# Optimization experiments

Hardware: AMD Instinct MI355X
Metric: run time of the kernel (lower is better)

The kernel has to match this reference:

```python
import jax, jax.numpy as jnp
import numpy as np

N_NODES = 50000
N_EDGES = 600000
D = 128
BN_EPS = 1e-5


def _linear_init(key, fan_in, fan_out):
    # torch nn.Linear default: U(-1/sqrt(fan_in), 1/sqrt(fan_in)) for W and b
    kw, kb = jax.random.split(key)
    bound = 1.0 / np.sqrt(fan_in)
    W = jax.random.uniform(kw, (fan_in, fan_out), minval=-bound, maxval=bound, dtype=jnp.float32)
    b = jax.random.uniform(kb, (fan_out,), minval=-bound, maxval=bound, dtype=jnp.float32)
    return W, b


def setup_inputs() -> dict:
    key = jax.random.key(0)
    ks = jax.random.split(key, 8)
    x = jax.random.normal(ks[0], (N_NODES, D), dtype=jnp.float32)
    edge_index = jax.random.randint(ks[1], (2, N_EDGES), 0, N_NODES, dtype=jnp.int32)
    edge_attr = jax.random.normal(ks[2], (N_EDGES, D), dtype=jnp.float32)
    # MLP: [2D, D, D, D] -> Linear(2D,D)+SiLU+BN, Linear(D,D)+SiLU+BN, Linear(D,D)
    W1, b1 = _linear_init(ks[3], 2 * D, D)
    W2, b2 = _linear_init(ks[4], D, D)
    W3, b3 = _linear_init(ks[5], D, D)
    g1 = jnp.ones((D,), jnp.float32); be1 = jnp.zeros((D,), jnp.float32)
    g2 = jnp.ones((D,), jnp.float32); be2 = jnp.zeros((D,), jnp.float32)
    return {"x": x, "edge_index": edge_index, "edge_attr": edge_attr,
            "W1": W1, "b1": b1, "g1": g1, "be1": be1,
            "W2": W2, "b2": b2, "g2": g2, "be2": be2,
            "W3": W3, "b3": b3}


def _bn(h, gamma, beta):
    # BatchNorm1d in training mode: normalize with batch statistics (biased var)
    mean = jnp.mean(h, axis=0)
    var = jnp.var(h, axis=0)
    return (h - mean) * jax.lax.rsqrt(var + BN_EPS) * gamma + beta


def reference(x, edge_index, edge_attr, W1, b1, g1, be1, W2, b2, g2, be2, W3, b3):
    src = edge_index[0]
    # scatter_add over edges indexed by source node -> [N_NODES, D]
    agg = jax.ops.segment_sum(edge_attr, src, num_segments=x.shape[0])
    h = jnp.concatenate([x, agg], axis=1)  # [N, 2D]
    h = _bn(jax.nn.silu(h @ W1 + b1), g1, be1)
    h = _bn(jax.nn.silu(h @ W2 + b2), g2, be2)
    return h @ W3 + b3
```

## Files before the change

### kernel.cpp

```cpp
#include <hip/hip_runtime.h>
#include <hip/hip_bf16.h>

#define D 128

typedef __attribute__((ext_vector_type(8))) short bfrag;
typedef __attribute__((ext_vector_type(4))) float facc;
typedef __attribute__((ext_vector_type(4))) unsigned int u32x4;
typedef __attribute__((ext_vector_type(2))) unsigned int u32x2;
typedef __attribute__((ext_vector_type(4))) float f32x4;

__device__ __forceinline__ facc mfma16(bfrag a, bfrag b, facc c) {
    return __builtin_amdgcn_mfma_f32_16x16x32_bf16(a, b, c, 0, 0, 0);
}
__device__ __forceinline__ unsigned int bf16_rn(float f) {
    unsigned int u = __float_as_uint(f);
    u += 0x7FFF + ((u >> 16) & 1);
    return u >> 16;
}
__device__ __forceinline__ float bf16_f(unsigned int h) {
    return __uint_as_float(h << 16);
}
__device__ __forceinline__ unsigned int packf(float v) {
    unsigned int hi = bf16_rn(v);
    unsigned int lo = bf16_rn(v - bf16_f(hi));
    return (hi << 16) | lo;
}

__global__ __launch_bounds__(256) void prep_kernel(
    const int* __restrict__ src, int* __restrict__ counts, int nedges,
    const float* __restrict__ x, unsigned int* __restrict__ xp, int n4,
    const float* __restrict__ W1, unsigned short* __restrict__ Wh,
    unsigned short* __restrict__ Wl, int eblk, int sblk) {
    int b = blockIdx.x;
    if (b < eblk) {
        int e = b * 256 + threadIdx.x;
        if (e < nedges) atomicAdd(&counts[src[e]], 1);
    } else if (b < eblk + sblk) {
        int i = (b - eblk) * 256 + threadIdx.x;
        if (i < n4) {
            float4 v = ((const float4*)x)[i];
            uint4 p;
            p.x = packf(v.x);
            p.y = packf(v.y);
            p.z = packf(v.z);
            p.w = packf(v.w);
            ((uint4*)xp)[i] = p;
        }
    } else {
        int j = b - eblk - sblk;
        int k = threadIdx.x;
        float w = W1[(size_t)k * D + j];
        unsigned int hi = bf16_rn(w);
        size_t o = (size_t)((k >> 3) * 128 + j) * 8 + (k & 7);
        Wh[o] = (unsigned short)hi;
        Wl[o] = (unsigned short)bf16_rn(w - bf16_f(hi));
    }
}

#define SCHUNK 2048
__global__ __launch_bounds__(256) void scan1_kernel(
    const int* __restrict__ counts, int* __restrict__ bsum, int n) {
    __shared__ int sd[256];
    const int tid = threadIdx.x;
    const int base = blockIdx.x * SCHUNK + tid * 8;
    int s = 0;
#pragma unroll
    for (int j = 0; j < 8; ++j) {
        int idx = base + j;
        if (idx < n) s += counts[idx];
    }
    sd[tid] = s;
    __syncthreads();
    for (int d2 = 128; d2; d2 >>= 1) {
        if (tid < d2) sd[tid] += sd[tid + d2];
        __syncthreads();
    }
    if (tid == 0) bsum[blockIdx.x] = sd[0];
}
__global__ void scan2_kernel(int* __restrict__ bsum, int nb) {
    int tid = threadIdx.x;
    int v = (tid < nb) ? bsum[tid] : 0;
#pragma unroll
    for (int d2 = 1; d2 < 64; d2 <<= 1) {
        int t = __shfl_up(v, d2);
        if (tid >= d2) v += t;
    }
    if (tid < nb) bsum[tid] = v;
}
__global__ __launch_bounds__(256) void scan3_kernel(
    const int* __restrict__ counts, const int* __restrict__ bsum,
    int* __restrict__ off, int* __restrict__ cur, int n) {
    __shared__ int sd[256];
    const int tid = threadIdx.x;
    const int base = blockIdx.x * SCHUNK + tid * 8;
    int loc[8];
    int s = 0;
#pragma unroll
    for (int j = 0; j < 8; ++j) {
        int idx = base + j;
        int c = (idx < n) ? counts[idx] : 0;
        loc[j] = c;
        s += c;
    }
    sd[tid] = s;
    __syncthreads();
#pragma unroll
    for (int d2 = 1; d2 < 256; d2 <<= 1) {
        int t = (tid >= d2) ? sd[tid - d2] : 0;
        __syncthreads();
        sd[tid] += t;
        __syncthreads();
    }
    int boff = (blockIdx.x == 0) ? 0 : bsum[blockIdx.x - 1];
    int pre = boff + sd[tid] - s;
#pragma unroll
    for (int j = 0; j < 8; ++j) {
        int idx = base + j;
        if (idx < n) {
            off[idx] = pre;
            cur[idx] = pre;
            pre += loc[j];
        }
    }
    if (tid == 255 && base + 8 >= n && n <= blockIdx.x * SCHUNK + SCHUNK)
        off[n] = boff + sd[255];
}

__global__ void fill_kernel(const int* __restrict__ src, int* __restrict__ cur,
                            int* __restrict__ eid, int nedges) {
    int e = blockIdx.x * 256 + threadIdx.x;
    if (e < nedges) {
        int slot = atomicAdd(&cur[src[e]], 1);
        eid[slot] = e;
    }
}

__global__ __launch_bounds__(256) void gather_kernel(
    const float* __restrict__ edge_attr, const int* __restrict__ eid,
    const int* __restrict__ off, unsigned int* __restrict__ aggp, int nnodes) {
    int node = blockIdx.x * 4 + (threadIdx.x >> 6);
    int lane = threadIdx.x & 63;
    if (node >= nnodes) return;
    const int h = lane >> 5;
    const int c = lane & 31;
    int i = off[node];
    const int e = off[node + 1];
    f32x4 acc = {0.f, 0.f, 0.f, 0.f};

    if (i < e && (i & 1)) {
        f32x4 v = __builtin_nontemporal_load(
            (const f32x4*)(edge_attr + (size_t)eid[i] * D) + c);
        if (h == 0) acc += v;
        ++i;
    }
    for (; i + 16 <= e; i += 16) {
        f32x4 v[8];
#pragma unroll
        for (int u = 0; u < 8; ++u) {
            int2 ep = *(const int2*)(eid + i + 2 * u);
            int row = h ? ep.y : ep.x;
            v[u] = __builtin_nontemporal_load(
                (const f32x4*)(edge_attr + (size_t)row * D) + c);
        }
#pragma unroll
        for (int u = 0; u < 8; ++u) acc += v[u];
    }
    for (; i + 4 <= e; i += 4) {
        int2 ep0 = *(const int2*)(eid + i);
        int2 ep1 = *(const int2*)(eid + i + 2);
        int r0 = h ? ep0.y : ep0.x;
        int r1 = h ? ep1.y : ep1.x;
        f32x4 v0 = __builtin_nontemporal_load(
            (const f32x4*)(edge_attr + (size_t)r0 * D) + c);
        f32x4 v1 = __builtin_nontemporal_load(
            (const f32x4*)(edge_attr + (size_t)r1 * D) + c);
        acc += v0;
        acc += v1;
    }
    for (; i + 2 <= e; i += 2) {
        int2 ep = *(const int2*)(eid + i);
        int row = h ? ep.y : ep.x;
        acc += __builtin_nontemporal_load(
            (const f32x4*)(edge_attr + (size_t)row * D) + c);
    }
    if (i < e) {
        f32x4 v = __builtin_nontemporal_load(
            (const f32x4*)(edge_attr + (size_t)eid[i] * D) + c);
        if (h == 0) acc += v;
    }
#pragma unroll
    for (int r = 0; r < 4; ++r) acc[r] += __shfl_xor(acc[r], 32);
    if (h == 0) {
        u32x4 p;
#pragma unroll
        for (int r = 0; r < 4; ++r) p[r] = packf(acc[r]);
        *((u32x4*)(aggp + (size_t)node * D) + c) = p;
    }
}

__global__ void fold_kernel(const float* __restrict__ sum,
                            const float* __restrict__ sq,
                            const float* __restrict__ gamma,
                            const float* __restrict__ beta,
                            const float* __restrict__ W,
                            const float* __restrict__ b,
                            unsigned short* __restrict__ Wh,
                            unsigned short* __restrict__ Wl,
                            float* __restrict__ bf, float invM) {
    int j = blockIdx.x;
    int k = threadIdx.x;
    float mean = sum[k] * invM;
    float var = sq[k] * invM - mean * mean;
    float scale = gamma[k] * rsqrtf(var + 1e-5f);
    float shift = beta[k] - mean * scale;
    float w = W[k * D + j];
    float wf = scale * w;
    unsigned int hi = bf16_rn(wf);
    size_t o = (size_t)((k >> 3) * 128 + j) * 8 + (k & 7);
    Wh[o] = (unsigned short)hi;
    Wl[o] = (unsigned short)bf16_rn(wf - bf16_f(hi));
    float v = shift * w;
#pragma unroll
    for (int of = 32; of; of >>= 1) v += __shfl_down(v, of);
    __shared__ float ws2[2];
    if ((k & 63) == 0) ws2[k >> 6] = v;
    __syncthreads();
    if (k == 0) bf[j] = b[j] + ws2[0] + ws2[1];
}

template <int K, bool SILU, bool STATS, bool PACKOUT>
__global__ __launch_bounds__(256, 2) void gemm_mfma(
    const unsigned int* __restrict__ A0, const unsigned int* __restrict__ A1,
    const unsigned short* __restrict__ Wh,
    const unsigned short* __restrict__ Wl,
    const float* __restrict__ bias, unsigned int* __restrict__ Cp,
    float* __restrict__ Cf, float* __restrict__ gsum,
    float* __restrict__ gsq, int M) {
    constexpr int NS = K / 32;
    const int tid = threadIdx.x;
    const int w = tid >> 6;
    const int l = tid & 63;
    const int lr = l & 15;
    const int lk = l >> 4;
    const int row0 = blockIdx.x * 128 + w * 32;

    facc acc[2][8];
#pragma unroll
    for (int rt = 0; rt < 2; ++rt)
#pragma unroll
        for (int ct = 0; ct < 8; ++ct)
#pragma unroll
            for (int r = 0; r < 4; ++r) acc[rt][ct][r] = 0.f;

    for (int s = 0; s < NS; ++s) {
        const int kb = s * 32 + lk * 8;
        bfrag ah[2], al[2];
#pragma unroll
        for (int rt = 0; rt < 2; ++rt) {
            const int arow = row0 + rt * 16 + lr;
            const unsigned int* As = A0;
            int kk = kb;
            if (K == 256 && s >= 4) { As = A1; kk = kb - 128; }
            u32x4 q0 = {0u, 0u, 0u, 0u}, q1 = {0u, 0u, 0u, 0u};
            if (arow < M) {
                const u32x4* p = (const u32x4*)(As + (size_t)arow * D + kk);
                q0 = p[0];
                q1 = p[1];
            }
            unsigned int ua[8] = {q0.x, q0.y, q0.z, q0.w,
                                  q1.x, q1.y, q1.z, q1.w};
            u32x4 uh, ul;
#pragma unroll
            for (int r = 0; r < 4; ++r) {
                uh[r] = __builtin_amdgcn_perm(ua[2 * r + 1], ua[2 * r],
                                              0x07060302u);
                ul[r] = __builtin_amdgcn_perm(ua[2 * r + 1], ua[2 * r],
                                              0x05040100u);
            }
            ah[rt] = __builtin_bit_cast(bfrag, uh);
            al[rt] = __builtin_bit_cast(bfrag, ul);
        }
        bfrag bh[8], bl[8];
        const int fb = (s * 4 + lk) * 128;
#pragma unroll
        for (int ct = 0; ct < 8; ++ct) {
            size_t o = (size_t)(fb + ct * 16 + lr) * 8;
            bh[ct] = *(const bfrag*)(Wh + o);
            bl[ct] = *(const bfrag*)(Wl + o);
        }
#pragma unroll
        for (int rt = 0; rt < 2; ++rt)
#pragma unroll
            for (int ct = 0; ct < 8; ++ct)
                acc[rt][ct] = mfma16(ah[rt], bh[ct], acc[rt][ct]);
#pragma unroll
        for (int rt = 0; rt < 2; ++rt)
#pragma unroll
            for (int ct = 0; ct < 8; ++ct)
                acc[rt][ct] = mfma16(ah[rt], bl[ct], acc[rt][ct]);
#pragma unroll
        for (int rt = 0; rt < 2; ++rt)
#pragma unroll
            for (int ct = 0; ct < 8; ++ct)
                acc[rt][ct] = mfma16(al[rt], bh[ct], acc[rt][ct]);
    }

    __shared__ float sred[2][4][128];
#pragma unroll
    for (int ct = 0; ct < 8; ++ct) {
        const int col = ct * 16 + lr;
        const float bj = bias[col];
        float s = 0.f, q = 0.f;
#pragma unroll
        for (int rt = 0; rt < 2; ++rt) {
            const int base = row0 + rt * 16 + lk * 4;
#pragma unroll
            for (int r = 0; r < 4; ++r) {
                int crow = base + r;
                if (crow < M) {
                    float v = acc[rt][ct][r] + bj;
                    if (SILU) v = v / (1.0f + __expf(-v));
                    if (PACKOUT) Cp[(size_t)crow * D + col] = packf(v);
                    else         Cf[(size_t)crow * D + col] = v;
                    if (STATS) { s += v; q += v * v; }
                }
            }
        }
        if (STATS) {
            s += __shfl_xor(s, 16);
            s += __shfl_xor(s, 32);
            q += __shfl_xor(q, 16);
            q += __shfl_xor(q, 32);
            if (lk == 0) {
                sred[0][w][col] = s;
                sred[1][w][col] = q;
            }
        }
    }
    if (STATS) {
        __syncthreads();
        if (tid < 128) {
            float v = sred[0][0][tid] + sred[0][1][tid] + sred[0][2][tid] +
                      sred[0][3][tid];
            unsafeAtomicAdd(&gsum[tid], v);
        } else {
            int c = tid - 128;
            float v = sred[1][0][c] + sred[1][1][c] + sred[1][2][c] +
                      sred[1][3][c];
            unsafeAtomicAdd(&gsq[c], v);
        }
    }
}

extern "C" void kernel_launch(void* const* d_in, const int* in_sizes, int n_in,
                              void* d_out, int out_size, void* d_ws,
                              size_t ws_size, hipStream_t stream) {
    const float* x     = (const float*)d_in[0];
    const int*   eidx  = (const int*)d_in[1];
    const float* eattr = (const float*)d_in[2];
    const float* W1  = (const float*)d_in[3];
    const float* b1  = (const float*)d_in[4];
    const float* g1  = (const float*)d_in[5];
    const float* be1 = (const float*)d_in[6];
    const float* W2  = (const float*)d_in[7];
    const float* b2  = (const float*)d_in[8];
    const float* g2  = (const float*)d_in[9];
    const float* be2 = (const float*)d_in[10];
    const float* W3  = (const float*)d_in[11];
    const float* b3  = (const float*)d_in[12];

    const int M = in_sizes[0] / D;
    const int E = in_sizes[1] / 2;
    const int* srcIdx = eidx;

    unsigned int* wsu = (unsigned int*)d_ws;
    unsigned int* aggp = wsu;
    unsigned int* xp   = aggp + (size_t)M * D;
    unsigned int* h1p  = xp + (size_t)M * D;
    unsigned int* h2p  = h1p + (size_t)M * D;
    int* counts = (int*)(h2p + (size_t)M * D);
    float* sum1 = (float*)(counts + M);
    float* sq1  = sum1 + D;
    float* sum2 = sq1 + D;
    float* sq2  = sum2 + D;
    float* b2f  = sq2 + D;
    float* b3f  = b2f + D;
    int* off    = (int*)(b3f + D);
    int* cur    = off + M + 4;
    int* eid    = cur + M;
    int* bsum   = eid + E;
    unsigned short* W1h = (unsigned short*)(bsum + 64);
    unsigned short* W1l = W1h + 256 * D;
    unsigned short* W2h = W1l + 256 * D;
    unsigned short* W2l = W2h + D * D;
    unsigned short* W3h = W2l + D * D;
    unsigned short* W3l = W3h + D * D;

    float* out = (float*)d_out;

    (void)hipMemsetAsync(counts, 0, ((size_t)M + 4 * D) * sizeof(int), stream);

    const int eblk = (E + 255) / 256;
    const int sblk = (M * 32 + 255) / 256;
    prep_kernel<<<eblk + sblk + 128, 256, 0, stream>>>(
        srcIdx, counts, E, x, xp, M * 32, W1, W1h, W1l, eblk, sblk);

    const int nb = (M + SCHUNK - 1) / SCHUNK;
    scan1_kernel<<<nb, 256, 0, stream>>>(counts, bsum, M);
    scan2_kernel<<<1, 64, 0, stream>>>(bsum, nb);
    scan3_kernel<<<nb, 256, 0, stream>>>(counts, bsum, off, cur, M);
    fill_kernel<<<eblk, 256, 0, stream>>>(srcIdx, cur, eid, E);

    gather_kernel<<<(M + 3) / 4, 256, 0, stream>>>(eattr, eid, off, aggp, M);

    int nblk = (M + 127) / 128;
    gemm_mfma<256, true, true, true><<<nblk, 256, 0, stream>>>(
        xp, aggp, W1h, W1l, b1, h1p, nullptr, sum1, sq1, M);
    fold_kernel<<<D, D, 0, stream>>>(sum1, sq1, g1, be1, W2, b2, W2h, W2l,
                                     b2f, 1.0f / (float)M);
    gemm_mfma<128, true, true, true><<<nblk, 256, 0, stream>>>(
        h1p, nullptr, W2h, W2l, b2f, h2p, nullptr, sum2, sq2, M);
    fold_kernel<<<D, D, 0, stream>>>(sum2, sq2, g2, be2, W3, b3, W3h, W3l,
                                     b3f, 1.0f / (float)M);
    gemm_mfma<128, false, false, false><<<nblk, 256, 0, stream>>>(
        h2p, nullptr, W3h, W3l, b3f, nullptr, out, nullptr, nullptr, M);
}
```

Baseline: 241.0 us.

## Fuse three-pass scan into one kernel with grid barrier; merge x/W1 split into gather

Replaces the three separate scan kernels with a single kernel. Each block publishes its block sum, then spins on an atomic counter as a grid-wide barrier before computing its prefix offset. The x and W1 hi/lo splitting work moves out of the histogram launch and into the gather kernel launch, so the histogram kernel stays lean and the split work runs alongside the gather. This removes two kernel launches. The spin barrier relies on all 25 blocks being co-resident, which holds here but is not guaranteed in general.

```diff
diff --git a/kernel.cpp b/kernel.cpp
--- a/kernel.cpp
+++ b/kernel.cpp
@@ -6,7 +6,6 @@
 typedef __attribute__((ext_vector_type(8))) short bfrag;
 typedef __attribute__((ext_vector_type(4))) float facc;
 typedef __attribute__((ext_vector_type(4))) unsigned int u32x4;
-typedef __attribute__((ext_vector_type(2))) unsigned int u32x2;
 typedef __attribute__((ext_vector_type(4))) float f32x4;
 
 __device__ __forceinline__ facc mfma16(bfrag a, bfrag b, facc c) {
@@ -26,17 +25,144 @@
     return (hi << 16) | lo;
 }
 
-__global__ __launch_bounds__(256) void prep_kernel(
-    const int* __restrict__ src, int* __restrict__ counts, int nedges,
+__global__ __launch_bounds__(256) void hist_kernel(
+    const int* __restrict__ src, int* __restrict__ counts, int nedges) {
+    int e = blockIdx.x * 256 + threadIdx.x;
+    if (e < nedges) atomicAdd(&counts[src[e]], 1);
+}
+
+#define SCHUNK 2048
+__global__ __launch_bounds__(256) void scanF_kernel(
+    const int* __restrict__ counts, int* __restrict__ bsum,
+    int* __restrict__ ctr, int* __restrict__ off, int* __restrict__ cur,
+    int n, int nbk) {
+    __shared__ int sd[256];
+    __shared__ int sbase;
+    const int tid = threadIdx.x;
+    const int b = blockIdx.x;
+    const int base = b * SCHUNK + tid * 8;
+    int loc[8];
+    int s = 0;
+#pragma unroll
+    for (int j = 0; j < 8; ++j) {
+        int idx = base + j;
+        int c = (idx < n) ? counts[idx] : 0;
+        loc[j] = c;
+        s += c;
+    }
+    sd[tid] = s;
+    __syncthreads();
+#pragma unroll
+    for (int d2 = 1; d2 < 256; d2 <<= 1) {
+        int t = (tid >= d2) ? sd[tid - d2] : 0;
+        __syncthreads();
+        sd[tid] += t;
+        __syncthreads();
+    }
+    if (tid == 0) {
+        atomicExch(&bsum[b], sd[255]);
+        __threadfence();
+        atomicAdd(ctr, 1);
+        while (atomicAdd(ctr, 0) < nbk) __builtin_amdgcn_s_sleep(8);
+    }
+    __syncthreads();
+    if (tid < 64) {
+        int t = (tid < b) ? atomicAdd(&bsum[tid], 0) : 0;
+#pragma unroll
+        for (int o = 32; o; o >>= 1) t += __shfl_down(t, o);
+        if (tid == 0) sbase = t;
+    }
+    __syncthreads();
+    int pre = sbase + sd[tid] - s;
+#pragma unroll
+    for (int j = 0; j < 8; ++j) {
+        int idx = base + j;
+        if (idx < n) {
+            off[idx] = pre;
+            cur[idx] = pre;
+            pre += loc[j];
+        }
+    }
+    if (b == nbk - 1 && tid == 0) off[n] = sbase + sd[255];
+}
+
+__global__ void fill_kernel(const int* __restrict__ src, int* __restrict__ cur,
+                            int* __restrict__ eid, int nedges) {
+    int e = blockIdx.x * 256 + threadIdx.x;
+    if (e < nedges) {
+        int slot = atomicAdd(&cur[src[e]], 1);
+        eid[slot] = e;
+    }
+}
+
+__global__ __launch_bounds__(256) void gather_split_kernel(
+    const float* __restrict__ edge_attr, const int* __restrict__ eid,
+    const int* __restrict__ off, unsigned int* __restrict__ aggp, int nnodes,
     const float* __restrict__ x, unsigned int* __restrict__ xp, int n4,
     const float* __restrict__ W1, unsigned short* __restrict__ Wh,
-    unsigned short* __restrict__ Wl, int eblk, int sblk) {
-    int b = blockIdx.x;
-    if (b < eblk) {
-        int e = b * 256 + threadIdx.x;
-        if (e < nedges) atomicAdd(&counts[src[e]], 1);
-    } else if (b < eblk + sblk) {
-        int i = (b - eblk) * 256 + threadIdx.x;
+    unsigned short* __restrict__ Wl, int gblk, int sblk) {
+    const int b = blockIdx.x;
+    if (b < gblk) {
+        int node = b * 4 + (threadIdx.x >> 6);
+        int lane = threadIdx.x & 63;
+        if (node >= nnodes) return;
+        const int h = lane >> 5;
+        const int c = lane & 31;
+        int i = off[node];
+        const int e = off[node + 1];
+        f32x4 acc = {0.f, 0.f, 0.f, 0.f};
+
+        if (i < e && (i & 1)) {
+            f32x4 v = __builtin_nontemporal_load(
+                (const f32x4*)(edge_attr + (size_t)eid[i] * D) + c);
+            if (h == 0) acc += v;
+            ++i;
+        }
+        for (; i + 16 <= e; i += 16) {
+            f32x4 v[8];
+#pragma unroll
+            for (int u = 0; u < 8; ++u) {
+                int2 ep = *(const int2*)(eid + i + 2 * u);
+                int row = h ? ep.y : ep.x;
+                v[u] = __builtin_nontemporal_load(
+                    (const f32x4*)(edge_attr + (size_t)row * D) + c);
+            }
+#pragma unroll
+            for (int u = 0; u < 8; ++u) acc += v[u];
+        }
+        for (; i + 4 <= e; i += 4) {
+            int2 ep0 = *(const int2*)(eid + i);
+            int2 ep1 = *(const int2*)(eid + i + 2);
+            int r0 = h ? ep0.y : ep0.x;
+            int r1 = h ? ep1.y : ep1.x;
+            f32x4 v0 = __builtin_nontemporal_load(
+                (const f32x4*)(edge_attr + (size_t)r0 * D) + c);
+            f32x4 v1 = __builtin_nontemporal_load(
+                (const f32x4*)(edge_attr + (size_t)r1 * D) + c);
+            acc += v0;
+            acc += v1;
+        }
+        for (; i + 2 <= e; i += 2) {
+            int2 ep = *(const int2*)(eid + i);
+            int row = h ? ep.y : ep.x;
+            acc += __builtin_nontemporal_load(
+                (const f32x4*)(edge_attr + (size_t)row * D) + c);
+        }
+        if (i < e) {
+            f32x4 v = __builtin_nontemporal_load(
+                (const f32x4*)(edge_attr + (size_t)eid[i] * D) + c);
+            if (h == 0) acc += v;
+        }
+#pragma unroll
+        for (int r = 0; r < 4; ++r) acc[r] += __shfl_xor(acc[r], 32);
+        if (h == 0) {
+            u32x4 p;
+#pragma unroll
+            for (int r = 0; r < 4; ++r) p[r] = packf(acc[r]);
+            *((u32x4*)(aggp + (size_t)node * D) + c) = p;
+        }
+    } else if (b < gblk + sblk) {
+        int i = (b - gblk) * 256 + threadIdx.x;
         if (i < n4) {
             float4 v = ((const float4*)x)[i];
             uint4 p;
@@ -47,154 +173,13 @@
             ((uint4*)xp)[i] = p;
         }
     } else {
-        int j = b - eblk - sblk;
+        int j = b - gblk - sblk;
         int k = threadIdx.x;
         float w = W1[(size_t)k * D + j];
         unsigned int hi = bf16_rn(w);
         size_t o = (size_t)((k >> 3) * 128 + j) * 8 + (k & 7);
         Wh[o] = (unsigned short)hi;
         Wl[o] = (unsigned short)bf16_rn(w - bf16_f(hi));
-    }
-}
-
-#define SCHUNK 2048
-__global__ __launch_bounds__(256) void scan1_kernel(
-    const int* __restrict__ counts, int* __restrict__ bsum, int n) {
-    __shared__ int sd[256];
-    const int tid = threadIdx.x;
-    const int base = blockIdx.x * SCHUNK + tid * 8;
-    int s = 0;
-#pragma unroll
-    for (int j = 0; j < 8; ++j) {
-        int idx = base + j;
-        if (idx < n) s += counts[idx];
-    }
-    sd[tid] = s;
-    __syncthreads();
-    for (int d2 = 128; d2; d2 >>= 1) {
-        if (tid < d2) sd[tid] += sd[tid + d2];
-        __syncthreads();
-    }
-    if (tid == 0) bsum[blockIdx.x] = sd[0];
-}
-__global__ void scan2_kernel(int* __restrict__ bsum, int nb) {
-    int tid = threadIdx.x;
-    int v = (tid < nb) ? bsum[tid] : 0;
-#pragma unroll
-    for (int d2 = 1; d2 < 64; d2 <<= 1) {
-        int t = __shfl_up(v, d2);
-        if (tid >= d2) v += t;
-    }
-    if (tid < nb) bsum[tid] = v;
-}
-__global__ __launch_bounds__(256) void scan3_kernel(
-    const int* __restrict__ counts, const int* __restrict__ bsum,
-    int* __restrict__ off, int* __restrict__ cur, int n) {
-    __shared__ int sd[256];
-    const int tid = threadIdx.x;
-    const int base = blockIdx.x * SCHUNK + tid * 8;
-    int loc[8];
-    int s = 0;
-#pragma unroll
-    for (int j = 0; j < 8; ++j) {
-        int idx = base + j;
-        int c = (idx < n) ? counts[idx] : 0;
-        loc[j] = c;
-        s += c;
-    }
-    sd[tid] = s;
-    __syncthreads();
-#pragma unroll
-    for (int d2 = 1; d2 < 256; d2 <<= 1) {
-        int t = (tid >= d2) ? sd[tid - d2] : 0;
-        __syncthreads();
-        sd[tid] += t;
-        __syncthreads();
-    }
-    int boff = (blockIdx.x == 0) ? 0 : bsum[blockIdx.x - 1];
-    int pre = boff + sd[tid] - s;
-#pragma unroll
-    for (int j = 0; j < 8; ++j) {
-        int idx = base + j;
-        if (idx < n) {
-            off[idx] = pre;
-            cur[idx] = pre;
-            pre += loc[j];
-        }
-    }
-    if (tid == 255 && base + 8 >= n && n <= blockIdx.x * SCHUNK + SCHUNK)
-        off[n] = boff + sd[255];
-}
-
-__global__ void fill_kernel(const int* __restrict__ src, int* __restrict__ cur,
-                            int* __restrict__ eid, int nedges) {
-    int e = blockIdx.x * 256 + threadIdx.x;
-    if (e < nedges) {
-        int slot = atomicAdd(&cur[src[e]], 1);
-        eid[slot] = e;
-    }
-}
-
-__global__ __launch_bounds__(256) void gather_kernel(
-    const float* __restrict__ edge_attr, const int* __restrict__ eid,
-    const int* __restrict__ off, unsigned int* __restrict__ aggp, int nnodes) {
-    int node = blockIdx.x * 4 + (threadIdx.x >> 6);
-    int lane = threadIdx.x & 63;
-    if (node >= nnodes) return;
-    const int h = lane >> 5;
-    const int c = lane & 31;
-    int i = off[node];
-    const int e = off[node + 1];
-    f32x4 acc = {0.f, 0.f, 0.f, 0.f};
-
-    if (i < e && (i & 1)) {
-        f32x4 v = __builtin_nontemporal_load(
-            (const f32x4*)(edge_attr + (size_t)eid[i] * D) + c);
-        if (h == 0) acc += v;
-        ++i;
-    }
-    for (; i + 16 <= e; i += 16) {
-        f32x4 v[8];
-#pragma unroll
-        for (int u = 0; u < 8; ++u) {
-            int2 ep = *(const int2*)(eid + i + 2 * u);
-            int row = h ? ep.y : ep.x;
-            v[u] = __builtin_nontemporal_load(
-                (const f32x4*)(edge_attr + (size_t)row * D) + c);
-        }
-#pragma unroll
-        for (int u = 0; u < 8; ++u) acc += v[u];
-    }
-    for (; i + 4 <= e; i += 4) {
-        int2 ep0 = *(const int2*)(eid + i);
-        int2 ep1 = *(const int2*)(eid + i + 2);
-        int r0 = h ? ep0.y : ep0.x;
-        int r1 = h ? ep1.y : ep1.x;
-        f32x4 v0 = __builtin_nontemporal_load(
-            (const f32x4*)(edge_attr + (size_t)r0 * D) + c);
-        f32x4 v1 = __builtin_nontemporal_load(
-            (const f32x4*)(edge_attr + (size_t)r1 * D) + c);
-        acc += v0;
-        acc += v1;
-    }
-    for (; i + 2 <= e; i += 2) {
-        int2 ep = *(const int2*)(eid + i);
-        int row = h ? ep.y : ep.x;
-        acc += __builtin_nontemporal_load(
-            (const f32x4*)(edge_attr + (size_t)row * D) + c);
-    }
-    if (i < e) {
-        f32x4 v = __builtin_nontemporal_load(
-            (const f32x4*)(edge_attr + (size_t)eid[i] * D) + c);
-        if (h == 0) acc += v;
-    }
-#pragma unroll
-    for (int r = 0; r < 4; ++r) acc[r] += __shfl_xor(acc[r], 32);
-    if (h == 0) {
-        u32x4 p;
-#pragma unroll
-        for (int r = 0; r < 4; ++r) p[r] = packf(acc[r]);
-        *((u32x4*)(aggp + (size_t)node * D) + c) = p;
     }
 }
 
@@ -379,7 +364,8 @@
     unsigned int* h1p  = xp + (size_t)M * D;
     unsigned int* h2p  = h1p + (size_t)M * D;
     int* counts = (int*)(h2p + (size_t)M * D);
-    float* sum1 = (float*)(counts + M);
+    int* ctr    = counts + M;
+    float* sum1 = (float*)(ctr + 4);
     float* sq1  = sum1 + D;
     float* sum2 = sq1 + D;
     float* sq2  = sum2 + D;
@@ -398,20 +384,20 @@
 
     float* out = (float*)d_out;
 
-    (void)hipMemsetAsync(counts, 0, ((size_t)M + 4 * D) * sizeof(int), stream);
+    (void)hipMemsetAsync(counts, 0, ((size_t)M + 4 + 4 * D) * sizeof(int),
+                         stream);
 
     const int eblk = (E + 255) / 256;
+    hist_kernel<<<eblk, 256, 0, stream>>>(srcIdx, counts, E);
+
+    const int nbk = (M + SCHUNK - 1) / SCHUNK;
+    scanF_kernel<<<nbk, 256, 0, stream>>>(counts, bsum, ctr, off, cur, M, nbk);
+    fill_kernel<<<eblk, 256, 0, stream>>>(srcIdx, cur, eid, E);
+
+    const int gblk = (M + 3) / 4;
     const int sblk = (M * 32 + 255) / 256;
-    prep_kernel<<<eblk + sblk + 128, 256, 0, stream>>>(
-        srcIdx, counts, E, x, xp, M * 32, W1, W1h, W1l, eblk, sblk);
-
-    const int nb = (M + SCHUNK - 1) / SCHUNK;
-    scan1_kernel<<<nb, 256, 0, stream>>>(counts, bsum, M);
-    scan2_kernel<<<1, 64, 0, stream>>>(bsum, nb);
-    scan3_kernel<<<nb, 256, 0, stream>>>(counts, bsum, off, cur, M);
-    fill_kernel<<<eblk, 256, 0, stream>>>(srcIdx, cur, eid, E);
-
-    gather_kernel<<<(M + 3) / 4, 256, 0, stream>>>(eattr, eid, off, aggp, M);
+    gather_split_kernel<<<gblk + sblk + 128, 256, 0, stream>>>(
+        eattr, eid, off, aggp, M, x, xp, M * 32, W1, W1h, W1l, gblk, sblk);
 
     int nblk = (M + 127) / 128;
     gemm_mfma<256, true, true, true><<<nblk, 256, 0, stream>>>(
```

New measurement: 240.8 us. About the same (-0.1%).
